# Kernel tuning notes

Measured on AMD Instinct MI355X. Metric: run time of the kernel, lower is better.

Reference implementation:

```python
import jax, jax.numpy as jnp
import numpy as np

N_NODES = 20000
N_EDGES = 320000
N_GRAPHS = 64
NEG_SLOPE = 0.2


def gat_conv(h, src, dst, a_src, a_dst, n_nodes):
    # h: [N, H, C] transformed node features; src/dst: [E] with self loops
    al_s = jnp.sum(h * a_src, axis=-1)  # [N, H]
    al_d = jnp.sum(h * a_dst, axis=-1)  # [N, H]
    e = jax.nn.leaky_relu(al_s[src] + al_d[dst], NEG_SLOPE)  # [E, H]
    m = jax.ops.segment_max(e, dst, num_segments=n_nodes)  # [N, H]
    ex = jnp.exp(e - m[dst])
    denom = jax.ops.segment_sum(ex, dst, num_segments=n_nodes)
    alpha = ex / denom[dst]  # [E, H] segment softmax over incoming edges
    # weighted scatter-aggregate of source features
    out = jax.ops.segment_sum(alpha[:, :, None] * h[src], dst, num_segments=n_nodes)
    return out  # [N, H, C]


def setup_inputs() -> dict:
    key = jax.random.key(0)
    ks = jax.random.split(key, 12)
    x = jax.random.normal(ks[0], (N_NODES, 3), dtype=jnp.float32)
    edge_index = jax.random.randint(ks[1], (2, N_EDGES), 0, N_NODES, dtype=jnp.int64)
    batch = jnp.sort(jax.random.randint(ks[2], (N_NODES,), 0, N_GRAPHS, dtype=jnp.int64))
    H1, C1 = 8, 8
    s = lambda fan_in: 1.0 / np.sqrt(fan_in)
    W1 = jax.random.normal(ks[3], (3, H1 * C1), dtype=jnp.float32) * s(3)
    a_src1 = jax.random.normal(ks[4], (H1, C1), dtype=jnp.float32) * s(C1)
    a_dst1 = jax.random.normal(ks[5], (H1, C1), dtype=jnp.float32) * s(C1)
    b1 = jnp.zeros((H1 * C1,), dtype=jnp.float32)
    W2 = jax.random.normal(ks[6], (H1 * C1, 512), dtype=jnp.float32) * s(H1 * C1)
    a_src2 = jax.random.normal(ks[7], (1, 512), dtype=jnp.float32) * s(512)
    a_dst2 = jax.random.normal(ks[8], (1, 512), dtype=jnp.float32) * s(512)
    b2 = jnp.zeros((512,), dtype=jnp.float32)
    Wo = jax.random.normal(ks[9], (512, 512), dtype=jnp.float32) * s(512)
    bo = jnp.zeros((512,), dtype=jnp.float32)
    return {"x": x, "edge_index": edge_index, "batch": batch,
            "W1": W1, "a_src1": a_src1, "a_dst1": a_dst1, "b1": b1,
            "W2": W2, "a_src2": a_src2, "a_dst2": a_dst2, "b2": b2,
            "Wo": Wo, "bo": bo}


def reference(x, edge_index, batch, W1, a_src1, a_dst1, b1,
              W2, a_src2, a_dst2, b2, Wo, bo):
    n = x.shape[0]
    loop = jnp.arange(n, dtype=edge_index.dtype)
    src = jnp.concatenate([edge_index[0], loop])
    dst = jnp.concatenate([edge_index[1], loop])
    # layer 1: 8 heads, concat
    h1 = (x @ W1).reshape(n, 8, 8)
    o1 = gat_conv(h1, src, dst, a_src1, a_dst1, n).reshape(n, 64) + b1
    o1 = jax.nn.elu(o1)
    # layer 2: 1 head, concat=False (mean over the single head)
    h2 = (o1 @ W2).reshape(n, 1, 512)
    o2 = gat_conv(h2, src, dst, a_src2, a_dst2, n)[:, 0, :] + b2
    o2 = jax.nn.elu(o2)
    # global mean pool per graph
    sums = jax.ops.segment_sum(o2, batch, num_segments=N_GRAPHS)
    cnt = jax.ops.segment_sum(jnp.ones((n,), dtype=o2.dtype), batch, num_segments=N_GRAPHS)
    pooled = sums / jnp.maximum(cnt, 1.0)[:, None]
    return pooled @ Wo + bo  # [G, 512]
```

## Files before the change

### kernel.cpp

```cpp
#include <hip/hip_runtime.h>
#include <math.h>

#define NN 20000
#define NE 320000
#define NT 340000
#define NG 64
#define HB 1329
#define CB 128
#define AB 2

using short8  = __attribute__((ext_vector_type(8))) short;
using float4v = __attribute__((ext_vector_type(4))) float;

__device__ __forceinline__ float lrelu(float v) { return v > 0.f ? v : 0.2f * v; }
__device__ __forceinline__ float elu1(float v)  { return v > 0.f ? v : (expf(v) - 1.f); }
__device__ __forceinline__ float bflo(unsigned u) { return __uint_as_float(u << 16); }
__device__ __forceinline__ float bfhi(unsigned u) { return __uint_as_float(u & 0xFFFF0000u); }
__device__ __forceinline__ unsigned short f2bf(float f) {
    unsigned u = __float_as_uint(f);
    u += 0x7FFFu + ((u >> 16) & 1u);
    return (unsigned short)(u >> 16);
}
__device__ __forceinline__ float bf2f(unsigned short s) {
    return __uint_as_float(((unsigned)s) << 16);
}

#define ACC8(ex, hv) \
    acc[0] = fmaf(ex, bflo(hv.x), acc[0]); \
    acc[1] = fmaf(ex, bfhi(hv.x), acc[1]); \
    acc[2] = fmaf(ex, bflo(hv.y), acc[2]); \
    acc[3] = fmaf(ex, bfhi(hv.y), acc[3]); \
    acc[4] = fmaf(ex, bflo(hv.z), acc[4]); \
    acc[5] = fmaf(ex, bfhi(hv.z), acc[5]); \
    acc[6] = fmaf(ex, bflo(hv.w), acc[6]); \
    acc[7] = fmaf(ex, bfhi(hv.w), acc[7]);

__device__ __forceinline__ int esrc(const int* ei, int e) { return e < NE ? ei[e] : (e - NE); }
__device__ __forceinline__ int edst(const int* ei, int e) { return e < NE ? ei[NE + e] : (e - NE); }

__global__ void k_prep(const int* __restrict__ ei, int* __restrict__ deg,
                       const float* __restrict__ W2, unsigned short* __restrict__ W2bfT,
                       const float* __restrict__ as2, const float* __restrict__ ad2,
                       float* __restrict__ a2ps, float* __restrict__ a2pd,
                       const float* __restrict__ x, const float* __restrict__ W1,
                       const float* __restrict__ as1, const float* __restrict__ ad1,
                       unsigned short* __restrict__ h1bf, float* __restrict__ al_s,
                       float* __restrict__ al_d) {
    int tid = threadIdx.x;
    int b = blockIdx.x;
    if (b < HB) {
        int t = b * 256 + tid;
        if (t < NE) atomicAdd(&deg[ei[NE + t]], 1);
        return;
    }
    if (b < HB + CB) {
        int t = (b - HB) * 256 + tid;
        int k = t & 63, n = t >> 6;
        W2bfT[t] = f2bf(W2[k * 512 + n]);
        return;
    }
    if (b < HB + CB + AB) {
        __shared__ float pp[4][64];
        const float* av = (b == HB + CB) ? as2 : ad2;
        float* outp     = (b == HB + CB) ? a2ps : a2pd;
        int k = tid & 63, seg = tid >> 6;
        float s = 0.f;
        for (int j = seg * 128; j < seg * 128 + 128; ++j)
            s = fmaf(W2[k * 512 + j], av[j], s);
        pp[seg][k] = s;
        __syncthreads();
        if (tid < 64) outp[tid] = pp[0][tid] + pp[1][tid] + pp[2][tid] + pp[3][tid];
        return;
    }
    int n = (b - HB - CB - AB) * 4 + (tid >> 6);
    int j = tid & 63;
    float x0 = x[n * 3 + 0], x1 = x[n * 3 + 1], x2 = x[n * 3 + 2];
    float v = fmaf(x0, W1[j], fmaf(x1, W1[64 + j], x2 * W1[128 + j]));
    h1bf[n * 64 + j] = f2bf(v);
    float ps = v * as1[j];
    float pd = v * ad1[j];
    for (int o = 4; o >= 1; o >>= 1) {
        ps += __shfl_xor(ps, o, 8);
        pd += __shfl_xor(pd, o, 8);
    }
    if ((j & 7) == 0) {
        al_s[n * 8 + (j >> 3)] = ps;
        al_d[n * 8 + (j >> 3)] = pd;
    }
}

__global__ void k_scan(const int* __restrict__ deg, const int* __restrict__ batch,
                       int* __restrict__ rowstart, int* __restrict__ cursor,
                       int* __restrict__ gstart) {
    __shared__ int part[1024];
    int t = threadIdx.x;
    int base = t * 20;
    int local[20];
    int s = 0;
    if (base < NN) {
#pragma unroll
        for (int i = 0; i < 20; ++i) { local[i] = deg[base + i] + 1; s += local[i]; }
    }
    part[t] = s;
    __syncthreads();
    for (int o = 1; o < 1024; o <<= 1) {
        int v = (t >= o) ? part[t - o] : 0;
        __syncthreads();
        part[t] += v;
        __syncthreads();
    }
    if (base < NN) {
        int run = (t == 0) ? 0 : part[t - 1];
#pragma unroll
        for (int i = 0; i < 20; ++i) {
            rowstart[base + i] = run;
            cursor[base + i] = run;
            run += local[i];
        }
    }
    if (t == 1023) rowstart[NN] = NT;
    if (t <= NG) {
        int lo = 0, hi = NN;
        while (lo < hi) {
            int mid = (lo + hi) >> 1;
            if (batch[mid] < t) lo = mid + 1; else hi = mid;
        }
        gstart[t] = lo;
    }
}

__global__ void k_scatter(const int* __restrict__ ei, int* __restrict__ cursor,
                          int* __restrict__ csr_src) {
    int t = blockIdx.x * blockDim.x + threadIdx.x;
    if (t >= NT) return;
    int d = edst(ei, t), s = esrc(ei, t);
    int pos = atomicAdd(&cursor[d], 1);
    csr_src[pos] = s;
}

__global__ void k_l1(const int* __restrict__ rowstart, const int* __restrict__ csr_src,
                     const float* __restrict__ al_s, const float* __restrict__ al_d,
                     const unsigned short* __restrict__ h1bf, const float* __restrict__ b1,
                     const float* __restrict__ a2ps, const float* __restrict__ a2pd,
                     unsigned short* __restrict__ o1bf, float* __restrict__ al_s2,
                     float* __restrict__ al_d2) {
    int nb = threadIdx.x >> 6;
    int n = blockIdx.x * 4 + nb;
    int lane = threadIdx.x & 63;
    int e8 = lane >> 3, c8 = lane & 7;
    int start = rowstart[n], end = rowstart[n + 1];
    int deg = end - start;
    float ald = al_d[n * 8 + c8];
    float acc[8] = {0.f, 0.f, 0.f, 0.f, 0.f, 0.f, 0.f, 0.f};
    float dsum = 0.f;
    for (int base = 0; base < deg; base += 16) {
        int slotA = base + e8;
        int slotB = base + 8 + e8;
        int sA = csr_src[start + (slotA < deg ? slotA : 0)];
        int sB = csr_src[start + (slotB < deg ? slotB : 0)];
        float exA = 0.f, exB = 0.f;
        if (slotA < deg) exA = __expf(lrelu(al_s[sA * 8 + c8] + ald));
        if (slotB < deg) exB = __expf(lrelu(al_s[sB * 8 + c8] + ald));
        dsum += exA + exB;
        uint4 hA = *(const uint4*)(h1bf + sA * 64 + c8 * 8);
        uint4 hB = *(const uint4*)(h1bf + sB * 64 + c8 * 8);
        ACC8(exA, hA);
        ACC8(exB, hB);
    }
#pragma unroll
    for (int o = 32; o >= 8; o >>= 1) {
#pragma unroll
        for (int k = 0; k < 8; ++k) acc[k] += __shfl_xor(acc[k], o, 64);
        dsum += __shfl_xor(dsum, o, 64);
    }
    if (e8 == 0) {
        float inv = 1.f / dsum;
        const float* bp = b1 + c8 * 8;
        float v[8];
#pragma unroll
        for (int k = 0; k < 8; ++k) v[k] = elu1(acc[k] * inv + bp[k]);
        uint4 pk;
        pk.x = (unsigned)f2bf(v[0]) | ((unsigned)f2bf(v[1]) << 16);
        pk.y = (unsigned)f2bf(v[2]) | ((unsigned)f2bf(v[3]) << 16);
        pk.z = (unsigned)f2bf(v[4]) | ((unsigned)f2bf(v[5]) << 16);
        pk.w = (unsigned)f2bf(v[6]) | ((unsigned)f2bf(v[7]) << 16);
        *(uint4*)(o1bf + n * 64 + c8 * 8) = pk;
        float ps = 0.f, pd = 0.f;
        const float* asp = a2ps + c8 * 8;
        const float* adp = a2pd + c8 * 8;
#pragma unroll
        for (int k = 0; k < 8; ++k) {
            ps = fmaf(v[k], asp[k], ps);
            pd = fmaf(v[k], adp[k], pd);
        }
        for (int o = 4; o >= 1; o >>= 1) {
            ps += __shfl_xor(ps, o, 8);
            pd += __shfl_xor(pd, o, 8);
        }
        if (c8 == 0) { al_s2[n] = ps; al_d2[n] = pd; }
    }
}

__global__ void k_l2gemm(const int* __restrict__ rowstart, const int* __restrict__ csr_src,
                         const float* __restrict__ al_s2, const float* __restrict__ al_d2,
                         const unsigned short* __restrict__ o1bf,
                         const unsigned short* __restrict__ W2bfT,
                         const float* __restrict__ b2, const int* __restrict__ batch,
                         float* __restrict__ sums) {
    __shared__ unsigned short lagg[16][72];
    int n0 = blockIdx.x * 16;
    int w = threadIdx.x >> 6, lane = threadIdx.x & 63;
    int e8 = lane >> 3, c8 = lane & 7;
#pragma unroll
    for (int i = 0; i < 2; ++i) {
        int r = w * 2 + i;
        int n = n0 + r;
        float ald = al_d2[n];
        int start = rowstart[n], end = rowstart[n + 1];
        int deg = end - start;
        float acc[8] = {0.f, 0.f, 0.f, 0.f, 0.f, 0.f, 0.f, 0.f};
        float dsum = 0.f;
        for (int base = 0; base < deg; base += 16) {
            int slotA = base + e8;
            int slotB = base + 8 + e8;
            int sA = csr_src[start + (slotA < deg ? slotA : 0)];
            int sB = csr_src[start + (slotB < deg ? slotB : 0)];
            float exA = 0.f, exB = 0.f;
            if (slotA < deg) exA = __expf(lrelu(al_s2[sA] + ald));
            if (slotB < deg) exB = __expf(lrelu(al_s2[sB] + ald));
            dsum += exA + exB;
            uint4 hA = *(const uint4*)(o1bf + sA * 64 + c8 * 8);
            uint4 hB = *(const uint4*)(o1bf + sB * 64 + c8 * 8);
            ACC8(exA, hA);
            ACC8(exB, hB);
        }
#pragma unroll
        for (int o = 32; o >= 8; o >>= 1) {
#pragma unroll
            for (int k = 0; k < 8; ++k) acc[k] += __shfl_xor(acc[k], o, 64);
            dsum += __shfl_xor(dsum, o, 64);
        }
        if (e8 == 0) {
            float inv = 1.f / dsum;
            uint4 pk;
            pk.x = (unsigned)f2bf(acc[0] * inv) | ((unsigned)f2bf(acc[1] * inv) << 16);
            pk.y = (unsigned)f2bf(acc[2] * inv) | ((unsigned)f2bf(acc[3] * inv) << 16);
            pk.z = (unsigned)f2bf(acc[4] * inv) | ((unsigned)f2bf(acc[5] * inv) << 16);
            pk.w = (unsigned)f2bf(acc[6] * inv) | ((unsigned)f2bf(acc[7] * inv) << 16);
            *(uint4*)&lagg[r][c8 * 8] = pk;
        }
    }
    __syncthreads();
    int mcol = lane & 15;
    int q = lane >> 4;
    short8 a0 = *(const short8*)&lagg[mcol][q * 8];
    short8 a1 = *(const short8*)&lagg[mcol][32 + q * 8];
    int gmin = batch[n0], gmax = batch[n0 + 15];
    int batchq[4];
#pragma unroll
    for (int r = 0; r < 4; ++r) batchq[r] = batch[n0 + q * 4 + r];
#pragma unroll
    for (int t = 0; t < 4; ++t) {
        int c = w * 64 + t * 16 + mcol;
        const unsigned short* bp = W2bfT + c * 64 + q * 8;
        short8 b0 = *(const short8*)bp;
        short8 b1v = *(const short8*)(bp + 32);
        float4v acc = {0.f, 0.f, 0.f, 0.f};
        acc = __builtin_amdgcn_mfma_f32_16x16x32_bf16(a0, b0, acc, 0, 0, 0);
        acc = __builtin_amdgcn_mfma_f32_16x16x32_bf16(a1, b1v, acc, 0, 0, 0);
        float bias = b2[c];
        float val[4];
#pragma unroll
        for (int r = 0; r < 4; ++r) val[r] = elu1(acc[r] + bias);
        for (int g = gmin; g <= gmax; ++g) {
            float s = 0.f;
#pragma unroll
            for (int r = 0; r < 4; ++r) s += (batchq[r] == g) ? val[r] : 0.f;
            s += __shfl_xor(s, 16, 64);
            s += __shfl_xor(s, 32, 64);
            if (q == 0) atomicAdd(&sums[g * 512 + c], s);
        }
    }
}

__global__ void k_final(const float* __restrict__ sums, const int* __restrict__ gstart,
                        const float* __restrict__ Wo, const float* __restrict__ bo,
                        float* __restrict__ out) {
    __shared__ float sp[512];
    int g = blockIdx.x >> 3;
    int j = (blockIdx.x & 7) * 64 + threadIdx.x;
    for (int k = threadIdx.x; k < 512; k += 64) sp[k] = sums[g * 512 + k];
    __syncthreads();
    float c = (float)(gstart[g + 1] - gstart[g]);
    float inv = 1.f / (c > 0.f ? c : 1.f);
    float acc = 0.f;
    for (int k = 0; k < 512; ++k) acc = fmaf(sp[k], Wo[k * 512 + j], acc);
    out[g * 512 + j] = fmaf(acc, inv, bo[j]);
}

extern "C" void kernel_launch(void* const* d_in, const int* in_sizes, int n_in,
                              void* d_out, int out_size, void* d_ws, size_t ws_size,
                              hipStream_t stream) {
    const float* x     = (const float*)d_in[0];
    const int*   ei    = (const int*)d_in[1];
    const int*   batch = (const int*)d_in[2];
    const float* W1    = (const float*)d_in[3];
    const float* as1   = (const float*)d_in[4];
    const float* ad1   = (const float*)d_in[5];
    const float* b1    = (const float*)d_in[6];
    const float* W2    = (const float*)d_in[7];
    const float* as2   = (const float*)d_in[8];
    const float* ad2   = (const float*)d_in[9];
    const float* b2    = (const float*)d_in[10];
    const float* Wo    = (const float*)d_in[11];
    const float* bo    = (const float*)d_in[12];
    float* out = (float*)d_out;

    float* w = (float*)d_ws;
    unsigned short* h1bf  = (unsigned short*)(w + 0);
    float* al_s1 = w + 640000;
    float* al_d1 = w + 800000;
    unsigned short* o1bf  = (unsigned short*)(w + 960000);
    unsigned short* W2bfT = (unsigned short*)(w + 1600000);
    float* a2ps  = w + 1616384;
    float* a2pd  = w + 1616448;
    float* al_s2 = w + 1616512;
    float* al_d2 = w + 1636512;
    int*   rowstart = (int*)(w + 1656512);
    int*   cursor   = (int*)(w + 1676516);
    int*   csr_src  = (int*)(w + 1696516);
    int*   gstart   = (int*)(w + 2036516);
    int*   deg      = (int*)(w + 2036584);
    float* sums     = w + 2056584;

    hipMemsetAsync(w + 2036584, 0, (size_t)(20000 + 32768) * 4, stream);

    k_prep   <<<HB + CB + AB + NN / 4, 256, 0, stream>>>(ei, deg, W2, W2bfT, as2, ad2,
                                                         a2ps, a2pd, x, W1, as1, ad1,
                                                         h1bf, al_s1, al_d1);
    k_scan   <<<1, 1024, 0, stream>>>(deg, batch, rowstart, cursor, gstart);
    k_scatter<<<HB, 256, 0, stream>>>(ei, cursor, csr_src);
    k_l1     <<<NN / 4, 256, 0, stream>>>(rowstart, csr_src, al_s1, al_d1, h1bf, b1,
                                          a2ps, a2pd, o1bf, al_s2, al_d2);
    k_l2gemm <<<NN / 16, 512, 0, stream>>>(rowstart, csr_src, al_s2, al_d2, o1bf,
                                           W2bfT, b2, batch, sums);
    k_final  <<<NG * 8, 64, 0, stream>>>(sums, gstart, Wo, bo, out);
}
```

Measured before the change: 194.9 us.

## Process two nodes per wave in GAT aggregation, tile W2 transpose, fold sums zeroing

New measurement: 200.9 us. 1.03x slower.

```diff
diff --git a/kernel.cpp b/kernel.cpp
--- a/kernel.cpp
+++ b/kernel.cpp
@@ -6,7 +6,7 @@
 #define NT 340000
 #define NG 64
 #define HB 1329
-#define CB 128
+#define CB 8
 #define AB 2
 
 using short8  = __attribute__((ext_vector_type(8))) short;
@@ -25,15 +25,15 @@
     return __uint_as_float(((unsigned)s) << 16);
 }
 
-#define ACC8(ex, hv) \
-    acc[0] = fmaf(ex, bflo(hv.x), acc[0]); \
-    acc[1] = fmaf(ex, bfhi(hv.x), acc[1]); \
-    acc[2] = fmaf(ex, bflo(hv.y), acc[2]); \
-    acc[3] = fmaf(ex, bfhi(hv.y), acc[3]); \
-    acc[4] = fmaf(ex, bflo(hv.z), acc[4]); \
-    acc[5] = fmaf(ex, bfhi(hv.z), acc[5]); \
-    acc[6] = fmaf(ex, bflo(hv.w), acc[6]); \
-    acc[7] = fmaf(ex, bfhi(hv.w), acc[7]);
+#define ACC8(A, ex, hv) \
+    A[0] = fmaf(ex, bflo(hv.x), A[0]); \
+    A[1] = fmaf(ex, bfhi(hv.x), A[1]); \
+    A[2] = fmaf(ex, bflo(hv.y), A[2]); \
+    A[3] = fmaf(ex, bfhi(hv.y), A[3]); \
+    A[4] = fmaf(ex, bflo(hv.z), A[4]); \
+    A[5] = fmaf(ex, bfhi(hv.z), A[5]); \
+    A[6] = fmaf(ex, bflo(hv.w), A[6]); \
+    A[7] = fmaf(ex, bfhi(hv.w), A[7]);
 
 __device__ __forceinline__ int esrc(const int* ei, int e) { return e < NE ? ei[e] : (e - NE); }
 __device__ __forceinline__ int edst(const int* ei, int e) { return e < NE ? ei[NE + e] : (e - NE); }
@@ -54,9 +54,21 @@
         return;
     }
     if (b < HB + CB) {
-        int t = (b - HB) * 256 + tid;
-        int k = t & 63, n = t >> 6;
-        W2bfT[t] = f2bf(W2[k * 512 + n]);
+        __shared__ unsigned short tile[64][65];
+        int n0t = (b - HB) * 64;
+#pragma unroll
+        for (int r = 0; r < 16; ++r) {
+            int k = r * 4 + (tid >> 6);
+            int nl = tid & 63;
+            tile[k][nl] = f2bf(W2[k * 512 + n0t + nl]);
+        }
+        __syncthreads();
+#pragma unroll
+        for (int r = 0; r < 16; ++r) {
+            int nl = r * 4 + (tid >> 6);
+            int k = tid & 63;
+            W2bfT[(n0t + nl) * 64 + k] = tile[k][nl];
+        }
         return;
     }
     if (b < HB + CB + AB) {
@@ -91,9 +103,15 @@
 
 __global__ void k_scan(const int* __restrict__ deg, const int* __restrict__ batch,
                        int* __restrict__ rowstart, int* __restrict__ cursor,
-                       int* __restrict__ gstart) {
+                       int* __restrict__ gstart, float* __restrict__ sums) {
     __shared__ int part[1024];
     int t = threadIdx.x;
+    {
+        float4* sp = (float4*)sums;
+#pragma unroll
+        for (int i = 0; i < 8; ++i)
+            sp[t * 8 + i] = make_float4(0.f, 0.f, 0.f, 0.f);
+    }
     int base = t * 20;
     int local[20];
     int s = 0;
@@ -144,60 +162,88 @@
                      const float* __restrict__ a2ps, const float* __restrict__ a2pd,
                      unsigned short* __restrict__ o1bf, float* __restrict__ al_s2,
                      float* __restrict__ al_d2) {
-    int nb = threadIdx.x >> 6;
-    int n = blockIdx.x * 4 + nb;
-    int lane = threadIdx.x & 63;
+    int w = threadIdx.x >> 6, lane = threadIdx.x & 63;
     int e8 = lane >> 3, c8 = lane & 7;
-    int start = rowstart[n], end = rowstart[n + 1];
-    int deg = end - start;
-    float ald = al_d[n * 8 + c8];
-    float acc[8] = {0.f, 0.f, 0.f, 0.f, 0.f, 0.f, 0.f, 0.f};
-    float dsum = 0.f;
-    for (int base = 0; base < deg; base += 16) {
-        int slotA = base + e8;
-        int slotB = base + 8 + e8;
-        int sA = csr_src[start + (slotA < deg ? slotA : 0)];
-        int sB = csr_src[start + (slotB < deg ? slotB : 0)];
-        float exA = 0.f, exB = 0.f;
-        if (slotA < deg) exA = __expf(lrelu(al_s[sA * 8 + c8] + ald));
-        if (slotB < deg) exB = __expf(lrelu(al_s[sB * 8 + c8] + ald));
-        dsum += exA + exB;
-        uint4 hA = *(const uint4*)(h1bf + sA * 64 + c8 * 8);
-        uint4 hB = *(const uint4*)(h1bf + sB * 64 + c8 * 8);
-        ACC8(exA, hA);
-        ACC8(exB, hB);
+    int nA = blockIdx.x * 8 + w * 2;
+    int nB = nA + 1;
+    int stA = rowstart[nA], degA = rowstart[nA + 1] - stA;
+    int stB = rowstart[nB], degB = rowstart[nB + 1] - stB;
+    float aldA = al_d[nA * 8 + c8], aldB = al_d[nB * 8 + c8];
+    float accA[8] = {0.f, 0.f, 0.f, 0.f, 0.f, 0.f, 0.f, 0.f};
+    float accB[8] = {0.f, 0.f, 0.f, 0.f, 0.f, 0.f, 0.f, 0.f};
+    float dsA = 0.f, dsB = 0.f;
+    int dmax = degA > degB ? degA : degB;
+    for (int base = 0; base < dmax; base += 16) {
+        int s0 = base + e8, s1 = base + 8 + e8;
+        int iA0 = csr_src[stA + (s0 < degA ? s0 : 0)];
+        int iA1 = csr_src[stA + (s1 < degA ? s1 : 0)];
+        int iB0 = csr_src[stB + (s0 < degB ? s0 : 0)];
+        int iB1 = csr_src[stB + (s1 < degB ? s1 : 0)];
+        float eA0 = (s0 < degA) ? __expf(lrelu(al_s[iA0 * 8 + c8] + aldA)) : 0.f;
+        float eA1 = (s1 < degA) ? __expf(lrelu(al_s[iA1 * 8 + c8] + aldA)) : 0.f;
+        float eB0 = (s0 < degB) ? __expf(lrelu(al_s[iB0 * 8 + c8] + aldB)) : 0.f;
+        float eB1 = (s1 < degB) ? __expf(lrelu(al_s[iB1 * 8 + c8] + aldB)) : 0.f;
+        uint4 hA0 = *(const uint4*)(h1bf + iA0 * 64 + c8 * 8);
+        uint4 hA1 = *(const uint4*)(h1bf + iA1 * 64 + c8 * 8);
+        uint4 hB0 = *(const uint4*)(h1bf + iB0 * 64 + c8 * 8);
+        uint4 hB1 = *(const uint4*)(h1bf + iB1 * 64 + c8 * 8);
+        dsA += eA0 + eA1;
+        dsB += eB0 + eB1;
+        ACC8(accA, eA0, hA0);
+        ACC8(accA, eA1, hA1);
+        ACC8(accB, eB0, hB0);
+        ACC8(accB, eB1, hB1);
     }
 #pragma unroll
     for (int o = 32; o >= 8; o >>= 1) {
 #pragma unroll
-        for (int k = 0; k < 8; ++k) acc[k] += __shfl_xor(acc[k], o, 64);
-        dsum += __shfl_xor(dsum, o, 64);
+        for (int k = 0; k < 8; ++k) {
+            accA[k] += __shfl_xor(accA[k], o, 64);
+            accB[k] += __shfl_xor(accB[k], o, 64);
+        }
+        dsA += __shfl_xor(dsA, o, 64);
+        dsB += __shfl_xor(dsB, o, 64);
     }
     if (e8 == 0) {
-        float inv = 1.f / dsum;
+        float invA = 1.f / dsA, invB = 1.f / dsB;
         const float* bp = b1 + c8 * 8;
-        float v[8];
-#pragma unroll
-        for (int k = 0; k < 8; ++k) v[k] = elu1(acc[k] * inv + bp[k]);
-        uint4 pk;
-        pk.x = (unsigned)f2bf(v[0]) | ((unsigned)f2bf(v[1]) << 16);
-        pk.y = (unsigned)f2bf(v[2]) | ((unsigned)f2bf(v[3]) << 16);
-        pk.z = (unsigned)f2bf(v[4]) | ((unsigned)f2bf(v[5]) << 16);
-        pk.w = (unsigned)f2bf(v[6]) | ((unsigned)f2bf(v[7]) << 16);
-        *(uint4*)(o1bf + n * 64 + c8 * 8) = pk;
-        float ps = 0.f, pd = 0.f;
         const float* asp = a2ps + c8 * 8;
         const float* adp = a2pd + c8 * 8;
+        float vA[8], vB[8];
 #pragma unroll
         for (int k = 0; k < 8; ++k) {
-            ps = fmaf(v[k], asp[k], ps);
-            pd = fmaf(v[k], adp[k], pd);
+            vA[k] = elu1(accA[k] * invA + bp[k]);
+            vB[k] = elu1(accB[k] * invB + bp[k]);
+        }
+        uint4 pkA, pkB;
+        pkA.x = (unsigned)f2bf(vA[0]) | ((unsigned)f2bf(vA[1]) << 16);
+        pkA.y = (unsigned)f2bf(vA[2]) | ((unsigned)f2bf(vA[3]) << 16);
+        pkA.z = (unsigned)f2bf(vA[4]) | ((unsigned)f2bf(vA[5]) << 16);
+        pkA.w = (unsigned)f2bf(vA[6]) | ((unsigned)f2bf(vA[7]) << 16);
+        pkB.x = (unsigned)f2bf(vB[0]) | ((unsigned)f2bf(vB[1]) << 16);
+        pkB.y = (unsigned)f2bf(vB[2]) | ((unsigned)f2bf(vB[3]) << 16);
+        pkB.z = (unsigned)f2bf(vB[4]) | ((unsigned)f2bf(vB[5]) << 16);
+        pkB.w = (unsigned)f2bf(vB[6]) | ((unsigned)f2bf(vB[7]) << 16);
+        *(uint4*)(o1bf + nA * 64 + c8 * 8) = pkA;
+        *(uint4*)(o1bf + nB * 64 + c8 * 8) = pkB;
+        float psA = 0.f, pdA = 0.f, psB = 0.f, pdB = 0.f;
+#pragma unroll
+        for (int k = 0; k < 8; ++k) {
+            psA = fmaf(vA[k], asp[k], psA);
+            pdA = fmaf(vA[k], adp[k], pdA);
+            psB = fmaf(vB[k], asp[k], psB);
+            pdB = fmaf(vB[k], adp[k], pdB);
         }
         for (int o = 4; o >= 1; o >>= 1) {
-            ps += __shfl_xor(ps, o, 8);
-            pd += __shfl_xor(pd, o, 8);
-        }
-        if (c8 == 0) { al_s2[n] = ps; al_d2[n] = pd; }
+            psA += __shfl_xor(psA, o, 8);
+            pdA += __shfl_xor(pdA, o, 8);
+            psB += __shfl_xor(psB, o, 8);
+            pdB += __shfl_xor(pdB, o, 8);
+        }
+        if (c8 == 0) {
+            al_s2[nA] = psA; al_d2[nA] = pdA;
+            al_s2[nB] = psB; al_d2[nB] = pdB;
+        }
     }
 }
 
@@ -211,44 +257,59 @@
     int n0 = blockIdx.x * 16;
     int w = threadIdx.x >> 6, lane = threadIdx.x & 63;
     int e8 = lane >> 3, c8 = lane & 7;
-#pragma unroll
-    for (int i = 0; i < 2; ++i) {
-        int r = w * 2 + i;
-        int n = n0 + r;
-        float ald = al_d2[n];
-        int start = rowstart[n], end = rowstart[n + 1];
-        int deg = end - start;
-        float acc[8] = {0.f, 0.f, 0.f, 0.f, 0.f, 0.f, 0.f, 0.f};
-        float dsum = 0.f;
-        for (int base = 0; base < deg; base += 16) {
-            int slotA = base + e8;
-            int slotB = base + 8 + e8;
-            int sA = csr_src[start + (slotA < deg ? slotA : 0)];
-            int sB = csr_src[start + (slotB < deg ? slotB : 0)];
-            float exA = 0.f, exB = 0.f;
-            if (slotA < deg) exA = __expf(lrelu(al_s2[sA] + ald));
-            if (slotB < deg) exB = __expf(lrelu(al_s2[sB] + ald));
-            dsum += exA + exB;
-            uint4 hA = *(const uint4*)(o1bf + sA * 64 + c8 * 8);
-            uint4 hB = *(const uint4*)(o1bf + sB * 64 + c8 * 8);
-            ACC8(exA, hA);
-            ACC8(exB, hB);
-        }
-#pragma unroll
-        for (int o = 32; o >= 8; o >>= 1) {
-#pragma unroll
-            for (int k = 0; k < 8; ++k) acc[k] += __shfl_xor(acc[k], o, 64);
-            dsum += __shfl_xor(dsum, o, 64);
-        }
-        if (e8 == 0) {
-            float inv = 1.f / dsum;
-            uint4 pk;
-            pk.x = (unsigned)f2bf(acc[0] * inv) | ((unsigned)f2bf(acc[1] * inv) << 16);
-            pk.y = (unsigned)f2bf(acc[2] * inv) | ((unsigned)f2bf(acc[3] * inv) << 16);
-            pk.z = (unsigned)f2bf(acc[4] * inv) | ((unsigned)f2bf(acc[5] * inv) << 16);
-            pk.w = (unsigned)f2bf(acc[6] * inv) | ((unsigned)f2bf(acc[7] * inv) << 16);
-            *(uint4*)&lagg[r][c8 * 8] = pk;
-        }
+    int rA = w * 2, rB = rA + 1;
+    int nA = n0 + rA, nB = n0 + rB;
+    int stA = rowstart[nA], degA = rowstart[nA + 1] - stA;
+    int stB = rowstart[nB], degB = rowstart[nB + 1] - stB;
+    float aldA = al_d2[nA], aldB = al_d2[nB];
+    float accA[8] = {0.f, 0.f, 0.f, 0.f, 0.f, 0.f, 0.f, 0.f};
+    float accB[8] = {0.f, 0.f, 0.f, 0.f, 0.f, 0.f, 0.f, 0.f};
+    float dsA = 0.f, dsB = 0.f;
+    int dmax = degA > degB ? degA : degB;
+    for (int base = 0; base < dmax; base += 16) {
+        int s0 = base + e8, s1 = base + 8 + e8;
+        int iA0 = csr_src[stA + (s0 < degA ? s0 : 0)];
+        int iA1 = csr_src[stA + (s1 < degA ? s1 : 0)];
+        int iB0 = csr_src[stB + (s0 < degB ? s0 : 0)];
+        int iB1 = csr_src[stB + (s1 < degB ? s1 : 0)];
+        float eA0 = (s0 < degA) ? __expf(lrelu(al_s2[iA0] + aldA)) : 0.f;
+        float eA1 = (s1 < degA) ? __expf(lrelu(al_s2[iA1] + aldA)) : 0.f;
+        float eB0 = (s0 < degB) ? __expf(lrelu(al_s2[iB0] + aldB)) : 0.f;
+        float eB1 = (s1 < degB) ? __expf(lrelu(al_s2[iB1] + aldB)) : 0.f;
+        uint4 hA0 = *(const uint4*)(o1bf + iA0 * 64 + c8 * 8);
+        uint4 hA1 = *(const uint4*)(o1bf + iA1 * 64 + c8 * 8);
+        uint4 hB0 = *(const uint4*)(o1bf + iB0 * 64 + c8 * 8);
+        uint4 hB1 = *(const uint4*)(o1bf + iB1 * 64 + c8 * 8);
+        dsA += eA0 + eA1;
+        dsB += eB0 + eB1;
+        ACC8(accA, eA0, hA0);
+        ACC8(accA, eA1, hA1);
+        ACC8(accB, eB0, hB0);
+        ACC8(accB, eB1, hB1);
+    }
+#pragma unroll
+    for (int o = 32; o >= 8; o >>= 1) {
+#pragma unroll
+        for (int k = 0; k < 8; ++k) {
+            accA[k] += __shfl_xor(accA[k], o, 64);
+            accB[k] += __shfl_xor(accB[k], o, 64);
+        }
+        dsA += __shfl_xor(dsA, o, 64);
+        dsB += __shfl_xor(dsB, o, 64);
+    }
+    if (e8 == 0) {
+        float invA = 1.f / dsA, invB = 1.f / dsB;
+        uint4 pkA, pkB;
+        pkA.x = (unsigned)f2bf(accA[0] * invA) | ((unsigned)f2bf(accA[1] * invA) << 16);
+        pkA.y = (unsigned)f2bf(accA[2] * invA) | ((unsigned)f2bf(accA[3] * invA) << 16);
+        pkA.z = (unsigned)f2bf(accA[4] * invA) | ((unsigned)f2bf(accA[5] * invA) << 16);
+        pkA.w = (unsigned)f2bf(accA[6] * invA) | ((unsigned)f2bf(accA[7] * invA) << 16);
+        pkB.x = (unsigned)f2bf(accB[0] * invB) | ((unsigned)f2bf(accB[1] * invB) << 16);
+        pkB.y = (unsigned)f2bf(accB[2] * invB) | ((unsigned)f2bf(accB[3] * invB) << 16);
+        pkB.z = (unsigned)f2bf(accB[4] * invB) | ((unsigned)f2bf(accB[5] * invB) << 16);
+        pkB.w = (unsigned)f2bf(accB[6] * invB) | ((unsigned)f2bf(accB[7] * invB) << 16);
+        *(uint4*)&lagg[rA][c8 * 8] = pkA;
+        *(uint4*)&lagg[rB][c8 * 8] = pkB;
     }
     __syncthreads();
     int mcol = lane & 15;
@@ -330,17 +391,17 @@
     int*   cursor   = (int*)(w + 1676516);
     int*   csr_src  = (int*)(w + 1696516);
     int*   gstart   = (int*)(w + 2036516);
-    int*   deg      = (int*)(w + 2036584);
-    float* sums     = w + 2056584;
-
-    hipMemsetAsync(w + 2036584, 0, (size_t)(20000 + 32768) * 4, stream);
+    float* sums     = w + 2036584;
+    int*   deg      = (int*)(w + 2069352);
+
+    hipMemsetAsync(w + 2069352, 0, (size_t)20000 * 4, stream);
 
     k_prep   <<<HB + CB + AB + NN / 4, 256, 0, stream>>>(ei, deg, W2, W2bfT, as2, ad2,
                                                          a2ps, a2pd, x, W1, as1, ad1,
                                                          h1bf, al_s1, al_d1);
-    k_scan   <<<1, 1024, 0, stream>>>(deg, batch, rowstart, cursor, gstart);
+    k_scan   <<<1, 1024, 0, stream>>>(deg, batch, rowstart, cursor, gstart, sums);
     k_scatter<<<HB, 256, 0, stream>>>(ei, cursor, csr_src);
-    k_l1     <<<NN / 4, 256, 0, stream>>>(rowstart, csr_src, al_s1, al_d1, h1bf, b1,
+    k_l1     <<<NN / 8, 256, 0, stream>>>(rowstart, csr_src, al_s1, al_d1, h1bf, b1,
                                           a2ps, a2pd, o1bf, al_s2, al_d2);
     k_l2gemm <<<NN / 16, 512, 0, stream>>>(rowstart, csr_src, al_s2, al_d2, o1bf,
                                            W2bfT, b2, batch, sums);
```
